# Performance work log

Hardware: AMD Instinct MI355X
Metric: run time of the kernel (lower is better)

## Reference

```python
import jax, jax.numpy as jnp
import numpy as np

D_MODEL = 1024
N_HEAD = 16
HEAD_DIM = D_MODEL // N_HEAD
BATCH = 2
SEQ = 2048


def setup_inputs() -> dict:
    key = jax.random.key(0)
    ks = jax.random.split(key, 5)
    std = np.sqrt(2.0 / (D_MODEL + D_MODEL)).astype(np.float32)
    return {
        "in_features": jax.random.normal(ks[0], (BATCH, SEQ, D_MODEL), dtype=jnp.float32),
        "Wq": jax.random.normal(ks[1], (D_MODEL, D_MODEL), dtype=jnp.float32) * std,
        "Wk": jax.random.normal(ks[2], (D_MODEL, D_MODEL), dtype=jnp.float32) * std,
        "Wv": jax.random.normal(ks[3], (D_MODEL, D_MODEL), dtype=jnp.float32) * std,
        "Wo": jax.random.normal(ks[4], (D_MODEL, D_MODEL), dtype=jnp.float32) * std,
    }


def reference(in_features, Wq, Wk, Wv, Wo):
    B, S, _ = in_features.shape
    # projections: x @ W (custom Linear stores weight as [in, out], no bias)
    q = (in_features @ Wq).reshape(B, S, N_HEAD, HEAD_DIM).transpose(0, 2, 1, 3)  # [B,H,S,Dh]
    k = (in_features @ Wk).reshape(B, S, N_HEAD, HEAD_DIM).transpose(0, 2, 1, 3)
    v = (in_features @ Wv).reshape(B, S, N_HEAD, HEAD_DIM).transpose(0, 2, 1, 3)
    scale = HEAD_DIM ** (-0.5)
    scores = jnp.einsum("bhqd,bhkd->bhqk", q, k) * scale  # [B,H,S,S]
    causal = jnp.tril(jnp.ones((S, S), dtype=bool))
    scores = jnp.where(causal, scores, -jnp.inf)
    attn = jax.nn.softmax(scores, axis=-1)
    ctx = jnp.einsum("bhqk,bhkd->bhqd", attn, v)  # [B,H,S,Dh]
    ctx = ctx.transpose(0, 2, 1, 3).reshape(B, S, D_MODEL)
    return ctx @ Wo
```

## Files before the change

### kernel.cpp

```cpp
#include <hip/hip_runtime.h>
#include <hip/hip_bf16.h>

#define DM 1024
#define NH 16
#define HD 64
#define B_ 2
#define S_ 2048
#define M_ (B_*S_)

typedef __attribute__((ext_vector_type(8))) short bf16x8;
typedef __attribute__((ext_vector_type(4))) float f32x4;
typedef __attribute__((ext_vector_type(4))) unsigned uint32x4;

__device__ __forceinline__ float bf2f(ushort u) {
  union { unsigned u32; float f; } c; c.u32 = ((unsigned)u) << 16; return c.f;
}
__device__ __forceinline__ ushort f2bf(float f) {
  union { float f; unsigned u32; } c; c.f = f;
  unsigned u = c.u32;
  unsigned r = (u + 0x7fffu + ((u >> 16) & 1u)) >> 16;
  return (ushort)r;
}
__device__ __forceinline__ unsigned fbits(float f) {
  union { float f; unsigned u; } c; c.f = f; return c.u;
}

__device__ __forceinline__ void async16(const ushort* g, ushort* l) {
  __builtin_amdgcn_global_load_lds((const __attribute__((address_space(1))) void*)g,
                                   (__attribute__((address_space(3))) void*)l, 16, 0, 0);
}

__device__ __forceinline__ void pswap32(unsigned& a, unsigned& b) {
  asm("v_permlane32_swap_b32 %0, %1" : "+v"(a), "+v"(b));
}
__device__ __forceinline__ void pswap16(unsigned& a, unsigned& b) {
  asm("v_permlane16_swap_b32 %0, %1" : "+v"(a), "+v"(b));
}

__global__ void cvt_prep(const float* __restrict__ x, const float* __restrict__ W0,
                         const float* __restrict__ W1, const float* __restrict__ W2,
                         const float* __restrict__ W3, ushort* __restrict__ wt,
                         ushort* __restrict__ xb) {
  __shared__ float tile[64][65];
  int z = blockIdx.z;
  int tx = threadIdx.x, ty = threadIdx.y;
  if (z == 4) {
    int tid = ty * 64 + tx;
    size_t base4 = ((size_t)blockIdx.y * 16 + blockIdx.x) * 4096;
    const float4* xv = (const float4*)x;
    ushort4* ov = (ushort4*)xb;
    #pragma unroll
    for (int k = 0; k < 16; ++k) {
      float4 v = xv[base4 + k * 256 + tid];
      ushort4 o;
      o.x = f2bf(v.x); o.y = f2bf(v.y); o.z = f2bf(v.z); o.w = f2bf(v.w);
      ov[base4 + k * 256 + tid] = o;
    }
    return;
  }
  const float* W = (z == 0) ? W0 : (z == 1) ? W1 : (z == 2) ? W2 : W3;
  ushort* Wt = wt + (size_t)z * (DM * DM);
  int c0 = blockIdx.x * 64, r0 = blockIdx.y * 64;
  #pragma unroll
  for (int i = ty; i < 64; i += 4) tile[i][tx] = W[(size_t)(r0 + i) * DM + c0 + tx];
  __syncthreads();
  #pragma unroll
  for (int i = ty; i < 64; i += 4) Wt[(size_t)(c0 + i) * DM + r0 + tx] = f2bf(tile[tx][i]);
}

template <int MODE, int BN>
__device__ __forceinline__ void gemm_body(const ushort* __restrict__ A,
                                          const ushort* __restrict__ Bt,
                                          ushort* __restrict__ Cb,
                                          float* __restrict__ Cf,
                                          ushort* As, ushort* Bs, ushort* Ts) {
  const int K = DM;
  constexpr int CN = BN / 32;
  int m0 = blockIdx.y * 128;
  int n0 = blockIdx.x * BN;
  int t = threadIdx.x;
  int lane = t & 63, wave = t >> 6;
  int wm = (wave >> 1) * 64, wn = (wave & 1) * (BN / 2);
  int lrow = lane & 15, quad = lane >> 4;

  int Ra = wave * 32;
  int Rb = wave * (BN / 4);
  int srow = lane >> 2, scol = (lane & 3) * 8;

  f32x4 acc[4][CN];
  #pragma unroll
  for (int r = 0; r < 4; ++r)
    #pragma unroll
    for (int c = 0; c < CN; ++c) acc[r][c] = (f32x4){0.f, 0.f, 0.f, 0.f};

  for (int k0 = 0; k0 < K; k0 += 32) {
    const ushort* ga = A + (size_t)(m0 + Ra + srow) * K + k0 + scol;
    const ushort* gb = Bt + (size_t)(n0 + Rb + srow) * K + k0 + scol;
    async16(ga,          As + Ra * 32);
    async16(ga + 16 * K, As + (Ra + 16) * 32);
    async16(gb,          Bs + Rb * 32);
    if (BN == 128) async16(gb + 16 * K, Bs + (Rb + 16) * 32);
    __syncthreads();

    bf16x8 af[4], bfr[CN];
    #pragma unroll
    for (int r = 0; r < 4; ++r)
      af[r] = *(const bf16x8*)(As + (wm + r * 16 + lrow) * 32 + quad * 8);
    #pragma unroll
    for (int c = 0; c < CN; ++c)
      bfr[c] = *(const bf16x8*)(Bs + (wn + c * 16 + lrow) * 32 + quad * 8);
    #pragma unroll
    for (int r = 0; r < 4; ++r)
      #pragma unroll
      for (int c = 0; c < CN; ++c)
        acc[r][c] = __builtin_amdgcn_mfma_f32_16x16x32_bf16(af[r], bfr[c], acc[r][c], 0, 0, 0);
    __syncthreads();
  }

  if constexpr (MODE == 2) {
    int bb = m0 >> 11;
    int s0base = m0 & 2047;
    #pragma unroll
    for (int H = 0; H < 2; ++H) {
      __syncthreads();
      if ((wave >> 1) == H) {
        #pragma unroll
        for (int r = 0; r < 4; ++r)
          #pragma unroll
          for (int c = 0; c < 4; ++c) {
            uint2 pk;
            pk.x = (unsigned)f2bf(acc[r][c][0]) | ((unsigned)f2bf(acc[r][c][1]) << 16);
            pk.y = (unsigned)f2bf(acc[r][c][2]) | ((unsigned)f2bf(acc[r][c][3]) << 16);
            *(uint2*)(Ts + (wn + c * 16 + lrow) * 72 + r * 16 + quad * 4) = pk;
          }
      }
      __syncthreads();
      #pragma unroll
      for (int i = 0; i < 4; ++i) {
        int id = t + i * 256;
        int nn = id >> 3, col = (id & 7) * 8;
        uint4 v = *(const uint4*)(Ts + nn * 72 + col);
        int h2 = (n0 >> 6) + (nn >> 6), d2 = nn & 63;
        size_t dst = (((size_t)(bb * NH + h2)) * HD + d2) * (size_t)S_ + s0base + H * 64 + col;
        *(uint4*)(Cb + dst) = v;
      }
    }
  } else {
    #pragma unroll
    for (int r = 0; r < 4; ++r) {
      #pragma unroll
      for (int c = 0; c < CN; ++c) {
        #pragma unroll
        for (int e = 0; e < 4; ++e) {
          int m = m0 + wm + r * 16 + quad * 4 + e;
          int n = n0 + wn + c * 16 + lrow;
          if (MODE == 0) {
            Cf[(size_t)m * DM + n] = acc[r][c][e];
          } else {
            int b = m >> 11, s = m & 2047, h = n >> 6, d = n & 63;
            Cb[(((size_t)(b * NH + h)) * S_ + s) * HD + d] = f2bf(acc[r][c][e]);
          }
        }
      }
    }
  }
}

__global__ __launch_bounds__(256, 3) void gemm_qkv(const ushort* __restrict__ A,
                                                   const ushort* __restrict__ wt,
                                                   ushort* __restrict__ qkv) {
  __shared__ __align__(16) ushort smem[9216];
  ushort* As = smem;
  ushort* Bs = smem + 4096;
  ushort* Ts = smem;
  int z = blockIdx.z;
  if (z < 2)
    gemm_body<1, 128>(A, wt + (size_t)z * (DM * DM), qkv + (size_t)z * ((size_t)M_ * DM),
                      nullptr, As, Bs, Ts);
  else
    gemm_body<2, 128>(A, wt + (size_t)2 * (DM * DM), qkv + (size_t)2 * ((size_t)M_ * DM),
                      nullptr, As, Bs, Ts);
}

__global__ __launch_bounds__(256, 3) void gemm_out(const ushort* __restrict__ A,
                                                   const ushort* __restrict__ wt,
                                                   float* __restrict__ C) {
  __shared__ __align__(16) ushort As[128 * 32];
  __shared__ __align__(16) ushort Bs[64 * 32];
  gemm_body<0, 64>(A, wt, nullptr, C, As, Bs, nullptr);
}

#define EXPC 0.18033688011f

struct AttnState {
  f32x4 o[4];
  float l;
};

template <bool MASKED>
__device__ __forceinline__ void attn_tile_compute(
    int q0, int kt, bf16x8 qf0, bf16x8 qf1,
    const bf16x8 kf0[4], const bf16x8 kf1[4],
    const bf16x8 vf0[4], const bf16x8 vf1[4],
    AttnState& st, int lrow, int quad) {
  f32x4 s[4];
  #pragma unroll
  for (int c = 0; c < 4; ++c) {
    f32x4 z = (f32x4){0.f, 0.f, 0.f, 0.f};
    z = __builtin_amdgcn_mfma_f32_16x16x32_bf16(kf0[c], qf0, z, 0, 0, 0);
    z = __builtin_amdgcn_mfma_f32_16x16x32_bf16(kf1[c], qf1, z, 0, 0, 0);
    s[c] = z;
  }
  int q = q0 + lrow;
  unsigned w0[4], w1[4];
  #pragma unroll
  for (int c = 0; c < 4; ++c) {
    float pv[4];
    #pragma unroll
    for (int e = 0; e < 4; ++e) {
      float v = __builtin_amdgcn_exp2f(s[c][e] * EXPC);
      if (MASKED) {
        int key = kt + c * 16 + quad * 4 + e;
        v = (key <= q) ? v : 0.f;
      }
      pv[e] = v;
      st.l += v;
    }
    w0[c] = __builtin_amdgcn_perm(fbits(pv[1]), fbits(pv[0]), 0x07060302u);
    w1[c] = __builtin_amdgcn_perm(fbits(pv[3]), fbits(pv[2]), 0x07060302u);
  }

  unsigned a0 = w0[0], b0 = w0[1]; pswap32(a0, b0); pswap16(a0, b0);
  unsigned a1 = w1[0], b1 = w1[1]; pswap32(a1, b1); pswap16(a1, b1);
  unsigned c0 = w0[2], d0 = w0[3]; pswap32(c0, d0); pswap16(c0, d0);
  unsigned c1 = w1[2], d1 = w1[3]; pswap32(c1, d1); pswap16(c1, d1);
  union { uint32x4 u; bf16x8 b; } P0, P1;
  P0.u = (uint32x4){a0, a1, b0, b1};
  P1.u = (uint32x4){c0, c1, d0, d1};

  #pragma unroll
  for (int dt = 0; dt < 4; ++dt) {
    st.o[dt] = __builtin_amdgcn_mfma_f32_16x16x32_bf16(P0.b, vf0[dt], st.o[dt], 0, 0, 0);
    st.o[dt] = __builtin_amdgcn_mfma_f32_16x16x32_bf16(P1.b, vf1[dt], st.o[dt], 0, 0, 0);
  }
}

__global__ __launch_bounds__(256, 2) void attn_mfma(const ushort* __restrict__ Q,
                                                    const ushort* __restrict__ Kmat,
                                                    const ushort* __restrict__ Vt,
                                                    ushort* __restrict__ ctx) {
  __shared__ __align__(16) ushort Ks[2][64 * 72];
  __shared__ __align__(16) ushort Vs[2][64 * 72];
  int t = threadIdx.x;
  int lane = t & 63, wave = t >> 6;
  int lrow = lane & 15, quad = lane >> 4;
  int bh = blockIdx.y;
  int p = blockIdx.x;
  int qt_lo = p, qt_hi = 31 - p;
  const ushort* Kb = Kmat + (size_t)bh * S_ * HD;
  const ushort* Vb = Vt + (size_t)bh * HD * S_;
  int b = bh >> 4, h = bh & 15;

  int r0 = t >> 3, s0 = (t & 7) * 8;
  int r1 = (t + 256) >> 3, s1 = s0;

  int q0_lo = qt_lo * 64 + wave * 16;
  int q0_hi = qt_hi * 64 + wave * 16;
  const ushort* Qlo = Q + ((size_t)bh * S_ + q0_lo) * HD;
  const ushort* Qhi = Q + ((size_t)bh * S_ + q0_hi) * HD;
  bf16x8 qlo0 = *(const bf16x8*)(Qlo + (size_t)lrow * HD + quad * 8);
  bf16x8 qlo1 = *(const bf16x8*)(Qlo + (size_t)lrow * HD + 32 + quad * 8);
  bf16x8 qhi0 = *(const bf16x8*)(Qhi + (size_t)lrow * HD + quad * 8);
  bf16x8 qhi1 = *(const bf16x8*)(Qhi + (size_t)lrow * HD + 32 + quad * 8);

  AttnState lo, hi;
  #pragma unroll
  for (int i = 0; i < 4; ++i) {
    lo.o[i] = (f32x4){0.f, 0.f, 0.f, 0.f}; hi.o[i] = (f32x4){0.f, 0.f, 0.f, 0.f};
  }
  lo.l = 0.f; hi.l = 0.f;

  int kend = qt_hi * 64;
  int lo_end = qt_lo * 64;

  {
    uint4 ka = *(const uint4*)(Kb + (size_t)r0 * HD + s0);
    uint4 kb2 = *(const uint4*)(Kb + (size_t)r1 * HD + s1);
    uint4 va = *(const uint4*)(Vb + (size_t)r0 * S_ + s0);
    uint4 vb2 = *(const uint4*)(Vb + (size_t)r1 * S_ + s1);
    *(uint4*)(Ks[0] + r0 * 72 + s0) = ka;
    *(uint4*)(Ks[0] + r1 * 72 + s1) = kb2;
    *(uint4*)(Vs[0] + r0 * 72 + s0) = va;
    *(uint4*)(Vs[0] + r1 * 72 + s1) = vb2;
  }
  __syncthreads();

  for (int kt = 0; kt <= kend; kt += 64) {
    int cur = (kt >> 6) & 1, nxt = cur ^ 1;
    bool has_next = (kt < kend);

    uint4 ka, kb2, va, vb2;
    if (has_next) {
      int ktn = kt + 64;
      ka  = *(const uint4*)(Kb + (size_t)(ktn + r0) * HD + s0);
      kb2 = *(const uint4*)(Kb + (size_t)(ktn + r1) * HD + s1);
      va  = *(const uint4*)(Vb + (size_t)r0 * S_ + ktn + s0);
      vb2 = *(const uint4*)(Vb + (size_t)r1 * S_ + ktn + s1);
    }

    bf16x8 kf0[4], kf1[4], vf0[4], vf1[4];
    #pragma unroll
    for (int c = 0; c < 4; ++c) {
      const ushort* kr = Ks[cur] + (c * 16 + lrow) * 72;
      kf0[c] = *(const bf16x8*)(kr + quad * 8);
      kf1[c] = *(const bf16x8*)(kr + 32 + quad * 8);
      const ushort* vr = Vs[cur] + (c * 16 + lrow) * 72;
      vf0[c] = *(const bf16x8*)(vr + quad * 8);
      vf1[c] = *(const bf16x8*)(vr + 32 + quad * 8);
    }

    if (kt < kend)
      attn_tile_compute<false>(q0_hi, kt, qhi0, qhi1, kf0, kf1, vf0, vf1, hi, lrow, quad);
    else
      attn_tile_compute<true>(q0_hi, kt, qhi0, qhi1, kf0, kf1, vf0, vf1, hi, lrow, quad);
    if (kt < lo_end)
      attn_tile_compute<false>(q0_lo, kt, qlo0, qlo1, kf0, kf1, vf0, vf1, lo, lrow, quad);
    else if (kt == lo_end)
      attn_tile_compute<true>(q0_lo, kt, qlo0, qlo1, kf0, kf1, vf0, vf1, lo, lrow, quad);

    if (has_next) {
      *(uint4*)(Ks[nxt] + r0 * 72 + s0) = ka;
      *(uint4*)(Ks[nxt] + r1 * 72 + s1) = kb2;
      *(uint4*)(Vs[nxt] + r0 * 72 + s0) = va;
      *(uint4*)(Vs[nxt] + r1 * 72 + s1) = vb2;
    }
    __syncthreads();
  }

  #pragma unroll
  for (int half = 0; half < 2; ++half) {
    AttnState& st = half ? hi : lo;
    int q0 = half ? q0_hi : q0_lo;
    float l = st.l;
    l += __shfl_xor(l, 16);
    l += __shfl_xor(l, 32);
    float rl = 1.0f / l;
    #pragma unroll
    for (int e = 0; e < 4; ++e) {
      float rinv = __shfl(rl, quad * 4 + e);
      int q = q0 + quad * 4 + e;
      #pragma unroll
      for (int dt = 0; dt < 4; ++dt)
        ctx[((size_t)b * S_ + q) * DM + h * HD + dt * 16 + lrow] = f2bf(st.o[dt][e] * rinv);
    }
  }
}

extern "C" void kernel_launch(void* const* d_in, const int* in_sizes, int n_in,
                              void* d_out, int out_size, void* d_ws, size_t ws_size,
                              hipStream_t stream) {
  const float* x  = (const float*)d_in[0];
  const float* Wq = (const float*)d_in[1];
  const float* Wk = (const float*)d_in[2];
  const float* Wv = (const float*)d_in[3];
  const float* Wo = (const float*)d_in[4];
  float* out = (float*)d_out;
  ushort* ws = (ushort*)d_ws;

  ushort* xb  = ws;
  ushort* wt  = xb + (size_t)M_ * DM;
  ushort* qkv = wt + (size_t)4 * DM * DM;
  ushort* ctx = qkv + (size_t)3 * M_ * DM;

  cvt_prep<<<dim3(16, 16, 5), dim3(64, 4), 0, stream>>>(x, Wq, Wk, Wv, Wo, wt, xb);
  gemm_qkv<<<dim3(DM / 128, M_ / 128, 3), 256, 0, stream>>>(xb, wt, qkv);
  attn_mfma<<<dim3(16, B_ * NH), 256, 0, stream>>>(qkv, qkv + (size_t)M_ * DM,
                                                   qkv + (size_t)2 * M_ * DM, ctx);
  gemm_out<<<dim3(DM / 64, M_ / 128), 256, 0, stream>>>(ctx, wt + (size_t)3 * DM * DM, out);
}
```

Measured before the change: 178.3 us.

## Split paired causal query tiles into one block per tile, longest first

Replaces the load-balanced pairing of a low and a high query tile per block with one block per 64-row query tile, giving 1024 blocks launched heaviest tiles first. Launch bounds go from 2 to 4 blocks per SIMD-occupancy hint so more blocks can be resident. This aims to expose more parallelism and lower per-block register use, relying on longest-first scheduling instead of pairing to balance causal work. In exchange, each K/V tile loaded into shared memory now feeds only one query tile instead of two, roughly doubling K/V traffic.

After: 218.1 us. 22.3% more time.

```diff
diff --git a/kernel.cpp b/kernel.cpp
--- a/kernel.cpp
+++ b/kernel.cpp
@@ -245,7 +245,7 @@
   }
 }
 
-__global__ __launch_bounds__(256, 2) void attn_mfma(const ushort* __restrict__ Q,
+__global__ __launch_bounds__(256, 4) void attn_mfma(const ushort* __restrict__ Q,
                                                     const ushort* __restrict__ Kmat,
                                                     const ushort* __restrict__ Vt,
                                                     ushort* __restrict__ ctx) {
@@ -254,9 +254,9 @@
   int t = threadIdx.x;
   int lane = t & 63, wave = t >> 6;
   int lrow = lane & 15, quad = lane >> 4;
-  int bh = blockIdx.y;
-  int p = blockIdx.x;
-  int qt_lo = p, qt_hi = 31 - p;
+  int n = blockIdx.x;
+  int qt = 31 - (n >> 5);
+  int bh = n & 31;
   const ushort* Kb = Kmat + (size_t)bh * S_ * HD;
   const ushort* Vb = Vt + (size_t)bh * HD * S_;
   int b = bh >> 4, h = bh & 15;
@@ -264,24 +264,17 @@
   int r0 = t >> 3, s0 = (t & 7) * 8;
   int r1 = (t + 256) >> 3, s1 = s0;
 
-  int q0_lo = qt_lo * 64 + wave * 16;
-  int q0_hi = qt_hi * 64 + wave * 16;
-  const ushort* Qlo = Q + ((size_t)bh * S_ + q0_lo) * HD;
-  const ushort* Qhi = Q + ((size_t)bh * S_ + q0_hi) * HD;
-  bf16x8 qlo0 = *(const bf16x8*)(Qlo + (size_t)lrow * HD + quad * 8);
-  bf16x8 qlo1 = *(const bf16x8*)(Qlo + (size_t)lrow * HD + 32 + quad * 8);
-  bf16x8 qhi0 = *(const bf16x8*)(Qhi + (size_t)lrow * HD + quad * 8);
-  bf16x8 qhi1 = *(const bf16x8*)(Qhi + (size_t)lrow * HD + 32 + quad * 8);
-
-  AttnState lo, hi;
-  #pragma unroll
-  for (int i = 0; i < 4; ++i) {
-    lo.o[i] = (f32x4){0.f, 0.f, 0.f, 0.f}; hi.o[i] = (f32x4){0.f, 0.f, 0.f, 0.f};
-  }
-  lo.l = 0.f; hi.l = 0.f;
-
-  int kend = qt_hi * 64;
-  int lo_end = qt_lo * 64;
+  int q0 = qt * 64 + wave * 16;
+  const ushort* Qp = Q + ((size_t)bh * S_ + q0) * HD;
+  bf16x8 qf0 = *(const bf16x8*)(Qp + (size_t)lrow * HD + quad * 8);
+  bf16x8 qf1 = *(const bf16x8*)(Qp + (size_t)lrow * HD + 32 + quad * 8);
+
+  AttnState st;
+  #pragma unroll
+  for (int i = 0; i < 4; ++i) st.o[i] = (f32x4){0.f, 0.f, 0.f, 0.f};
+  st.l = 0.f;
+
+  int kend = qt * 64;
 
   {
     uint4 ka = *(const uint4*)(Kb + (size_t)r0 * HD + s0);
@@ -320,13 +313,9 @@
     }
 
     if (kt < kend)
-      attn_tile_compute<false>(q0_hi, kt, qhi0, qhi1, kf0, kf1, vf0, vf1, hi, lrow, quad);
+      attn_tile_compute<false>(q0, kt, qf0, qf1, kf0, kf1, vf0, vf1, st, lrow, quad);
     else
-      attn_tile_compute<true>(q0_hi, kt, qhi0, qhi1, kf0, kf1, vf0, vf1, hi, lrow, quad);
-    if (kt < lo_end)
-      attn_tile_compute<false>(q0_lo, kt, qlo0, qlo1, kf0, kf1, vf0, vf1, lo, lrow, quad);
-    else if (kt == lo_end)
-      attn_tile_compute<true>(q0_lo, kt, qlo0, qlo1, kf0, kf1, vf0, vf1, lo, lrow, quad);
+      attn_tile_compute<true>(q0, kt, qf0, qf1, kf0, kf1, vf0, vf1, st, lrow, quad);
 
     if (has_next) {
       *(uint4*)(Ks[nxt] + r0 * 72 + s0) = ka;
@@ -337,10 +326,7 @@
     __syncthreads();
   }
 
-  #pragma unroll
-  for (int half = 0; half < 2; ++half) {
-    AttnState& st = half ? hi : lo;
-    int q0 = half ? q0_hi : q0_lo;
+  {
     float l = st.l;
     l += __shfl_xor(l, 16);
     l += __shfl_xor(l, 32);
@@ -374,7 +360,7 @@
 
   cvt_prep<<<dim3(16, 16, 5), dim3(64, 4), 0, stream>>>(x, Wq, Wk, Wv, Wo, wt, xb);
   gemm_qkv<<<dim3(DM / 128, M_ / 128, 3), 256, 0, stream>>>(xb, wt, qkv);
-  attn_mfma<<<dim3(16, B_ * NH), 256, 0, stream>>>(qkv, qkv + (size_t)M_ * DM,
-                                                   qkv + (size_t)2 * M_ * DM, ctx);
+  attn_mfma<<<dim3(32 * B_ * NH), 256, 0, stream>>>(qkv, qkv + (size_t)M_ * DM,
+                                                    qkv + (size_t)2 * M_ * DM, ctx);
   gemm_out<<<dim3(DM / 64, M_ / 128), 256, 0, stream>>>(ctx, wt + (size_t)3 * DM * DM, out);
 }
```
